# Performance work log

Hardware: AMD Instinct MI355X
Metric: run time of the kernel (lower is better)

The kernel has to match this reference:

```python
import jax, jax.numpy as jnp
import numpy as np

ROI = 7  # roi_size


def _conv1x1_softmax_fuse(a, b, w, bias):
    # a, b: (..., C, H, W); w: (2, 2C); bias: (2,)
    cat = jnp.concatenate([a, b], axis=-3)
    logits = jnp.einsum('oc,...chw->...ohw', w, cat) + bias[:, None, None]
    att = jax.nn.softmax(logits, axis=-3)
    return a * att[..., 0:1, :, :] + b * att[..., 1:2, :, :]


def _roi_align(feat, anchors):
    # torchvision RoIAlign (aligned=False, spatial_scale=1, sampling_ratio=-1).
    # Box width == ROI exactly -> bin size 1, adaptive grid = 1 sample per bin
    # at bin center: sample point = anchor - ROI/2 + (p + 0.5), p in [0, ROI).
    # feat: (C,H,W), anchors: (N,2) -> (N,C,ROI,ROI)
    C, H, W = feat.shape
    N = anchors.shape[0]
    half = ROI / 2.0
    offs = jnp.arange(ROI, dtype=feat.dtype) + 0.5
    sx = anchors[:, 0, None] - half + offs  # (N, ROI)
    sy = anchors[:, 1, None] - half + offs
    X = jnp.broadcast_to(sx[:, None, :], (N, ROI, ROI)).reshape(-1)  # pw fastest
    Y = jnp.broadcast_to(sy[:, :, None], (N, ROI, ROI)).reshape(-1)
    valid = (X >= -1.0) & (X <= W) & (Y >= -1.0) & (Y <= H)
    x = jnp.maximum(X, 0.0)
    y = jnp.maximum(Y, 0.0)
    x0 = jnp.floor(x).astype(jnp.int32)
    y0 = jnp.floor(y).astype(jnp.int32)
    xl = jnp.minimum(x0, W - 1)
    xh = jnp.minimum(x0 + 1, W - 1)
    yl = jnp.minimum(y0, H - 1)
    yh = jnp.minimum(y0 + 1, H - 1)
    lx = jnp.where(x0 >= W - 1, 0.0, x - xl)
    ly = jnp.where(y0 >= H - 1, 0.0, y - yl)
    hx, hy = 1.0 - lx, 1.0 - ly
    v = (feat[:, yl, xl] * (hy * hx) + feat[:, yl, xh] * (hy * lx)
         + feat[:, yh, xl] * (ly * hx) + feat[:, yh, xh] * (ly * lx))  # (C, P)
    v = jnp.where(valid, v, 0.0)
    return v.reshape(C, N, ROI, ROI).transpose(1, 0, 2, 3)


def _scatter_rois(base, rois, x0, y0):
    # sequential per-anchor overwrite of ROIxROI patches, matching torch loop order
    def step(m, args):
        roi, xx, yy = args
        return jax.lax.dynamic_update_slice(m, roi, (0, yy, xx)), None
    out, _ = jax.lax.scan(step, base, (rois, x0, y0))
    return out


def _forward(feat_rgb, feat_tir, a_rgb_c, a_tir_c, w_global, b_global, w_att, b_att):
    anchors_rgb = jax.lax.stop_gradient(a_rgb_c[..., :2])
    anchors_tir = jax.lax.stop_gradient(a_tir_c[..., :2])
    # GlobalFeatureFusion == per-pixel 1x1 conv + softmax-2 blend
    fused_global = _conv1x1_softmax_fuse(feat_rgb, feat_tir, w_global, b_global)
    rgb_rois = jax.vmap(_roi_align)(feat_rgb, anchors_rgb)  # (B,N,C,r,r)
    tir_rois = jax.vmap(_roi_align)(feat_tir, anchors_tir)
    fused_rois = _conv1x1_softmax_fuse(rgb_rois, tir_rois, w_att, b_att)
    fused_rois = jax.lax.stop_gradient(fused_rois)  # .detach() in fuse_rois_to_map
    H, W = feat_rgb.shape[2], feat_rgb.shape[3]
    half = ROI / 2.0
    x0 = jnp.clip(jnp.trunc(anchors_rgb[..., 0] - half).astype(jnp.int32), 0, W - ROI)
    y0 = jnp.clip(jnp.trunc(anchors_rgb[..., 1] - half).astype(jnp.int32), 0, H - ROI)
    return jax.vmap(_scatter_rois)(fused_global, fused_rois, x0, y0)


def setup_inputs():
    key = jax.random.key(0)
    ks = jax.random.split(key, 10)
    B, C, H, W, N = 8, 256, 128, 128, 128
    half = ROI / 2.0
    feat_rgb = jax.random.normal(ks[0], (B, C, H, W), dtype=jnp.float32)
    feat_tir = jax.random.normal(ks[1], (B, C, H, W), dtype=jnp.float32)

    def anchors(kx, ky, kc):
        ax = jax.random.uniform(kx, (B, N), minval=half, maxval=W - half)
        ay = jax.random.uniform(ky, (B, N), minval=half, maxval=H - half)
        cf = jax.random.uniform(kc, (B, N))
        return jnp.stack([ax, ay, cf], axis=-1).astype(jnp.float32)

    a_rgb = anchors(ks[2], ks[3], ks[4])
    a_tir = anchors(ks[5], ks[6], ks[7])
    w_global = jax.random.normal(ks[8], (2, 2 * C), dtype=jnp.float32) * 0.05
    b_global = jnp.zeros((2,), dtype=jnp.float32)
    w_att = jax.random.normal(ks[9], (2, 2 * C), dtype=jnp.float32) * 0.05
    b_att = jnp.zeros((2,), dtype=jnp.float32)
    return {"feat_rgb": feat_rgb, "feat_tir": feat_tir,
            "anchors_rgb_with_conf": a_rgb, "anchors_tir_with_conf": a_tir,
            "w_global": w_global, "b_global": b_global,
            "w_att": w_att, "b_att": b_att}


def reference(feat_rgb, feat_tir, anchors_rgb_with_conf, anchors_tir_with_conf,
              w_global, b_global, w_att, b_att):
    return _forward(feat_rgb, feat_tir, anchors_rgb_with_conf, anchors_tir_with_conf,
                    w_global, b_global, w_att, b_att)
```

## Files before the change

### kernel.cpp

```cpp
#include <hip/hip_runtime.h>
#include <math.h>

#define ROI 7
#define NC 256
#define TC 512
#define HH 128
#define WW 128
#define HW (HH * WW)

__global__ void init_owner_k(int* __restrict__ owner, int n) {
    int i = blockIdx.x * blockDim.x + threadIdx.x;
    if (i < n) owner[i] = -1;
}

__global__ void mark_owner_k(const float* __restrict__ anchors,
                             int* __restrict__ owner, int B, int N) {
    int i = blockIdx.x * blockDim.x + threadIdx.x;
    int total = B * N * 49;
    if (i >= total) return;
    int p = i % 49;
    int bn = i / 49;
    int n = bn % N;
    int b = bn / N;
    float ax = anchors[(size_t)(b * N + n) * 3 + 0];
    float ay = anchors[(size_t)(b * N + n) * 3 + 1];
    int x0 = (int)truncf(ax - 3.5f); x0 = min(max(x0, 0), WW - ROI);
    int y0 = (int)truncf(ay - 3.5f); y0 = min(max(y0, 0), HH - ROI);
    int x = x0 + (p % 7);
    int y = y0 + (p / 7);
    atomicMax(&owner[((size_t)b << 14) + (y << 7) + x], n);
}

__global__ __launch_bounds__(512, 4) void fuse_global_k(
        const float* __restrict__ rgb, const float* __restrict__ tir,
        const float* __restrict__ wg, const float* __restrict__ bg,
        const int* __restrict__ owner, float* __restrict__ out) {
    __shared__ float w[2 * TC];
    __shared__ float part0[64][9];
    __shared__ float part1[64][9];
    __shared__ float att[64];

    int tid = threadIdx.x;
    int px = tid & 63;
    int g  = tid >> 6;
    int b = blockIdx.x >> 8;
    int pix = ((blockIdx.x & 255) << 6) + px;

    for (int i = tid; i < 2 * TC; i += 512) w[i] = wg[i];

    bool act = owner[((size_t)b << 14) + pix] < 0;

    const float* pr = rgb + (((size_t)b * NC) << 14) + pix;
    const float* pt = tir + (((size_t)b * NC) << 14) + pix;
    int c0 = g << 5;

    __syncthreads();

    float vr[32], vt[32];
    if (act) {
        float l0 = 0.f, l1 = 0.f;
        #pragma unroll
        for (int i = 0; i < 32; ++i) {
            int c = c0 + i;
            vr[i] = pr[(size_t)c << 14];
            vt[i] = pt[(size_t)c << 14];
            l0 = fmaf(w[c],          vr[i], fmaf(w[NC + c],     vt[i], l0));
            l1 = fmaf(w[2 * NC + c], vr[i], fmaf(w[3 * NC + c], vt[i], l1));
        }
        part0[px][g] = l0;
        part1[px][g] = l1;
    }
    __syncthreads();
    if (g == 0 && act) {
        float L0 = bg[0], L1 = bg[1];
        #pragma unroll
        for (int s = 0; s < 8; ++s) { L0 += part0[px][s]; L1 += part1[px][s]; }
        float m = fmaxf(L0, L1);
        float e0 = expf(L0 - m), e1 = expf(L1 - m);
        att[px] = e0 / (e0 + e1);
    }
    __syncthreads();
    if (!act) return;

    float a0 = att[px];
    float* po = out + (((size_t)b * NC) << 14) + pix;
    #pragma unroll
    for (int i = 0; i < 32; ++i) {
        int c = c0 + i;
        po[(size_t)c << 14] = fmaf(a0, vr[i] - vt[i], vt[i]);
    }
}

struct Bilin { int o00, o01, o10, o11; float w00, w01, w10, w11; };

__device__ inline Bilin bilin_setup(float X, float Y) {
    Bilin r;
    bool valid = (X >= -1.0f) && (X <= (float)WW) && (Y >= -1.0f) && (Y <= (float)HH);
    float x = fmaxf(X, 0.0f), y = fmaxf(Y, 0.0f);
    int ix = (int)floorf(x), iy = (int)floorf(y);
    int xl = min(ix, WW - 1), xh = min(ix + 1, WW - 1);
    int yl = min(iy, HH - 1), yh = min(iy + 1, HH - 1);
    float lx = (ix >= WW - 1) ? 0.0f : x - (float)xl;
    float ly = (iy >= HH - 1) ? 0.0f : y - (float)yl;
    float hx = 1.0f - lx, hy = 1.0f - ly;
    r.o00 = (yl << 7) + xl; r.o01 = (yl << 7) + xh;
    r.o10 = (yh << 7) + xl; r.o11 = (yh << 7) + xh;
    float s = valid ? 1.0f : 0.0f;
    r.w00 = hy * hx * s; r.w01 = hy * lx * s;
    r.w10 = ly * hx * s; r.w11 = ly * lx * s;
    return r;
}

__device__ inline float bgather(const float* __restrict__ base, int c, const Bilin& bl) {
    const float* p = base + ((size_t)c << 14);
    return p[bl.o00] * bl.w00 + p[bl.o01] * bl.w01 +
           p[bl.o10] * bl.w10 + p[bl.o11] * bl.w11;
}

__global__ __launch_bounds__(512) void roi_scatter_k(
        const float* __restrict__ rgb, const float* __restrict__ tir,
        const float* __restrict__ a_rgb, const float* __restrict__ a_tir,
        const float* __restrict__ wa, const float* __restrict__ ba,
        const int* __restrict__ owner, float* __restrict__ out, int N, int B) {
    __shared__ float w[2 * TC];
    __shared__ float part0[64][9];
    __shared__ float part1[64][9];
    __shared__ float att0s[64];

    int bid = blockIdx.x;
    int b = (B - 1) - bid / N;
    int n = bid % N;
    for (int i = threadIdx.x; i < 2 * TC; i += 512) w[i] = wa[i];

    int p = threadIdx.x & 63;
    int g = threadIdx.x >> 6;
    int px = p % 7, py = p / 7;

    float axr = a_rgb[(size_t)(b * N + n) * 3 + 0];
    float ayr = a_rgb[(size_t)(b * N + n) * 3 + 1];
    float axt = a_tir[(size_t)(b * N + n) * 3 + 0];
    float ayt = a_tir[(size_t)(b * N + n) * 3 + 1];

    int x0 = (int)truncf(axr - 3.5f); x0 = min(max(x0, 0), WW - ROI);
    int y0 = (int)truncf(ayr - 3.5f); y0 = min(max(y0, 0), HH - ROI);
    int x = x0 + px, y = y0 + py;

    bool act = (p < 49);
    if (act) act = (owner[((size_t)b << 14) + (y << 7) + x] == n);

    Bilin br = bilin_setup(axr - 3.0f + (float)px, ayr - 3.0f + (float)py);
    Bilin bt = bilin_setup(axt - 3.0f + (float)px, ayt - 3.0f + (float)py);

    const float* rb = rgb + (((size_t)b * NC) << 14);
    const float* tb = tir + (((size_t)b * NC) << 14);

    __syncthreads();

    int c0 = g << 5;
    float vr[32], vt[32];
    if (act) {
        float l0 = 0.f, l1 = 0.f;
        #pragma unroll
        for (int i = 0; i < 32; ++i) {
            int c = c0 + i;
            vr[i] = bgather(rb, c, br);
            vt[i] = bgather(tb, c, bt);
            l0 = fmaf(w[c],          vr[i], fmaf(w[NC + c],     vt[i], l0));
            l1 = fmaf(w[2 * NC + c], vr[i], fmaf(w[3 * NC + c], vt[i], l1));
        }
        part0[p][g] = l0;
        part1[p][g] = l1;
    }
    __syncthreads();
    if (g == 0 && p < 49) {
        float L0 = ba[0], L1 = ba[1];
        #pragma unroll
        for (int s = 0; s < 8; ++s) { L0 += part0[p][s]; L1 += part1[p][s]; }
        float m = fmaxf(L0, L1);
        float e0 = expf(L0 - m), e1 = expf(L1 - m);
        att0s[p] = e0 / (e0 + e1);
    }
    __syncthreads();
    if (!act) return;

    float a0 = att0s[p];
    float* po = out + (((size_t)b * NC) << 14) + (y << 7) + x;
    #pragma unroll
    for (int i = 0; i < 32; ++i) {
        int c = c0 + i;
        po[(size_t)c << 14] = fmaf(a0, vr[i] - vt[i], vt[i]);
    }
}

extern "C" void kernel_launch(void* const* d_in, const int* in_sizes, int n_in,
                              void* d_out, int out_size, void* d_ws, size_t ws_size,
                              hipStream_t stream) {
    const float* frgb = (const float*)d_in[0];
    const float* ftir = (const float*)d_in[1];
    const float* argb = (const float*)d_in[2];
    const float* atir = (const float*)d_in[3];
    const float* wg   = (const float*)d_in[4];
    const float* bgp  = (const float*)d_in[5];
    const float* wa   = (const float*)d_in[6];
    const float* bap  = (const float*)d_in[7];
    float* out = (float*)d_out;

    int B = in_sizes[0] / (NC * HW);
    int N = in_sizes[2] / (B * 3);
    int npix = B * HW;

    int* owner = (int*)d_ws;

    init_owner_k<<<(npix + 255) / 256, 256, 0, stream>>>(owner, npix);
    mark_owner_k<<<(B * N * 49 + 255) / 256, 256, 0, stream>>>(argb, owner, B, N);
    fuse_global_k<<<npix / 64, 512, 0, stream>>>(frgb, ftir, wg, bgp, owner, out);
    roi_scatter_k<<<B * N, 512, 0, stream>>>(frgb, ftir, argb, atir, wa, bap,
                                             owner, out, N, B);
}
```

Measured before the change: 223.6 us.

## Merge global fuse and ROI scatter kernels into one interleaved launch

Combines the global 1x1 fusion kernel and the ROI scatter kernel into a single launch whose blocks are dispatched as either ROI or global-fuse work. When the fuse block count is twice the ROI count, ROI blocks are interleaved one in three, so the gather-heavy ROI blocks overlap with the streaming fuse blocks rather than running as a separate tail. This removes one kernel launch and the serialization between them. In exchange, the merged kernel loses the fuse kernel's min-blocks launch bound hint, which may change register allocation and occupancy.

```diff
diff --git a/kernel.cpp b/kernel.cpp
--- a/kernel.cpp
+++ b/kernel.cpp
@@ -31,66 +31,6 @@
     atomicMax(&owner[((size_t)b << 14) + (y << 7) + x], n);
 }
 
-__global__ __launch_bounds__(512, 4) void fuse_global_k(
-        const float* __restrict__ rgb, const float* __restrict__ tir,
-        const float* __restrict__ wg, const float* __restrict__ bg,
-        const int* __restrict__ owner, float* __restrict__ out) {
-    __shared__ float w[2 * TC];
-    __shared__ float part0[64][9];
-    __shared__ float part1[64][9];
-    __shared__ float att[64];
-
-    int tid = threadIdx.x;
-    int px = tid & 63;
-    int g  = tid >> 6;
-    int b = blockIdx.x >> 8;
-    int pix = ((blockIdx.x & 255) << 6) + px;
-
-    for (int i = tid; i < 2 * TC; i += 512) w[i] = wg[i];
-
-    bool act = owner[((size_t)b << 14) + pix] < 0;
-
-    const float* pr = rgb + (((size_t)b * NC) << 14) + pix;
-    const float* pt = tir + (((size_t)b * NC) << 14) + pix;
-    int c0 = g << 5;
-
-    __syncthreads();
-
-    float vr[32], vt[32];
-    if (act) {
-        float l0 = 0.f, l1 = 0.f;
-        #pragma unroll
-        for (int i = 0; i < 32; ++i) {
-            int c = c0 + i;
-            vr[i] = pr[(size_t)c << 14];
-            vt[i] = pt[(size_t)c << 14];
-            l0 = fmaf(w[c],          vr[i], fmaf(w[NC + c],     vt[i], l0));
-            l1 = fmaf(w[2 * NC + c], vr[i], fmaf(w[3 * NC + c], vt[i], l1));
-        }
-        part0[px][g] = l0;
-        part1[px][g] = l1;
-    }
-    __syncthreads();
-    if (g == 0 && act) {
-        float L0 = bg[0], L1 = bg[1];
-        #pragma unroll
-        for (int s = 0; s < 8; ++s) { L0 += part0[px][s]; L1 += part1[px][s]; }
-        float m = fmaxf(L0, L1);
-        float e0 = expf(L0 - m), e1 = expf(L1 - m);
-        att[px] = e0 / (e0 + e1);
-    }
-    __syncthreads();
-    if (!act) return;
-
-    float a0 = att[px];
-    float* po = out + (((size_t)b * NC) << 14) + pix;
-    #pragma unroll
-    for (int i = 0; i < 32; ++i) {
-        int c = c0 + i;
-        po[(size_t)c << 14] = fmaf(a0, vr[i] - vt[i], vt[i]);
-    }
-}
-
 struct Bilin { int o00, o01, o10, o11; float w00, w01, w10, w11; };
 
 __device__ inline Bilin bilin_setup(float X, float Y) {
@@ -117,78 +57,140 @@
            p[bl.o10] * bl.w10 + p[bl.o11] * bl.w11;
 }
 
-__global__ __launch_bounds__(512) void roi_scatter_k(
+__global__ __launch_bounds__(512) void fused_k(
         const float* __restrict__ rgb, const float* __restrict__ tir,
         const float* __restrict__ a_rgb, const float* __restrict__ a_tir,
+        const float* __restrict__ wg, const float* __restrict__ bg,
         const float* __restrict__ wa, const float* __restrict__ ba,
-        const int* __restrict__ owner, float* __restrict__ out, int N, int B) {
+        const int* __restrict__ owner, float* __restrict__ out,
+        int N, int nRoi, int nFuse) {
     __shared__ float w[2 * TC];
     __shared__ float part0[64][9];
     __shared__ float part1[64][9];
-    __shared__ float att0s[64];
+    __shared__ float att[64];
 
     int bid = blockIdx.x;
-    int b = (B - 1) - bid / N;
-    int n = bid % N;
-    for (int i = threadIdx.x; i < 2 * TC; i += 512) w[i] = wa[i];
-
-    int p = threadIdx.x & 63;
-    int g = threadIdx.x >> 6;
-    int px = p % 7, py = p / 7;
-
-    float axr = a_rgb[(size_t)(b * N + n) * 3 + 0];
-    float ayr = a_rgb[(size_t)(b * N + n) * 3 + 1];
-    float axt = a_tir[(size_t)(b * N + n) * 3 + 0];
-    float ayt = a_tir[(size_t)(b * N + n) * 3 + 1];
-
-    int x0 = (int)truncf(axr - 3.5f); x0 = min(max(x0, 0), WW - ROI);
-    int y0 = (int)truncf(ayr - 3.5f); y0 = min(max(y0, 0), HH - ROI);
-    int x = x0 + px, y = y0 + py;
-
-    bool act = (p < 49);
-    if (act) act = (owner[((size_t)b << 14) + (y << 7) + x] == n);
-
-    Bilin br = bilin_setup(axr - 3.0f + (float)px, ayr - 3.0f + (float)py);
-    Bilin bt = bilin_setup(axt - 3.0f + (float)px, ayt - 3.0f + (float)py);
-
-    const float* rb = rgb + (((size_t)b * NC) << 14);
-    const float* tb = tir + (((size_t)b * NC) << 14);
-
-    __syncthreads();
-
+    int tid = threadIdx.x;
+
+    bool isRoi;
+    int idx;
+    if (nFuse == 2 * nRoi) {
+        int q = bid / 3, r = bid - 3 * q;
+        isRoi = (r == 0);
+        idx = isRoi ? q : (bid - q - 1);
+    } else {
+        isRoi = (bid < nRoi);
+        idx = isRoi ? bid : (bid - nRoi);
+    }
+
+    int p  = tid & 63;
+    int g  = tid >> 6;
     int c0 = g << 5;
-    float vr[32], vt[32];
-    if (act) {
-        float l0 = 0.f, l1 = 0.f;
+
+    if (isRoi) {
+        int b = idx / N, n = idx % N;
+        for (int i = tid; i < 2 * TC; i += 512) w[i] = wa[i];
+
+        int px = p % 7, py = p / 7;
+
+        float axr = a_rgb[(size_t)(b * N + n) * 3 + 0];
+        float ayr = a_rgb[(size_t)(b * N + n) * 3 + 1];
+        float axt = a_tir[(size_t)(b * N + n) * 3 + 0];
+        float ayt = a_tir[(size_t)(b * N + n) * 3 + 1];
+
+        int x0 = (int)truncf(axr - 3.5f); x0 = min(max(x0, 0), WW - ROI);
+        int y0 = (int)truncf(ayr - 3.5f); y0 = min(max(y0, 0), HH - ROI);
+        int x = x0 + px, y = y0 + py;
+
+        bool act = (p < 49);
+        if (act) act = (owner[((size_t)b << 14) + (y << 7) + x] == n);
+
+        Bilin br = bilin_setup(axr - 3.0f + (float)px, ayr - 3.0f + (float)py);
+        Bilin bt = bilin_setup(axt - 3.0f + (float)px, ayt - 3.0f + (float)py);
+
+        const float* rb = rgb + (((size_t)b * NC) << 14);
+        const float* tb = tir + (((size_t)b * NC) << 14);
+
+        __syncthreads();
+
+        float vr[32], vt[32];
+        if (act) {
+            float l0 = 0.f, l1 = 0.f;
+            #pragma unroll
+            for (int i = 0; i < 32; ++i) {
+                int c = c0 + i;
+                vr[i] = bgather(rb, c, br);
+                vt[i] = bgather(tb, c, bt);
+                l0 = fmaf(w[c],          vr[i], fmaf(w[NC + c],     vt[i], l0));
+                l1 = fmaf(w[2 * NC + c], vr[i], fmaf(w[3 * NC + c], vt[i], l1));
+            }
+            part0[p][g] = l0;
+            part1[p][g] = l1;
+        }
+        __syncthreads();
+        if (g == 0 && p < 49) {
+            float L0 = ba[0], L1 = ba[1];
+            #pragma unroll
+            for (int s = 0; s < 8; ++s) { L0 += part0[p][s]; L1 += part1[p][s]; }
+            float m = fmaxf(L0, L1);
+            float e0 = expf(L0 - m), e1 = expf(L1 - m);
+            att[p] = e0 / (e0 + e1);
+        }
+        __syncthreads();
+        if (!act) return;
+
+        float a0 = att[p];
+        float* po = out + (((size_t)b * NC) << 14) + (y << 7) + x;
         #pragma unroll
         for (int i = 0; i < 32; ++i) {
             int c = c0 + i;
-            vr[i] = bgather(rb, c, br);
-            vt[i] = bgather(tb, c, bt);
-            l0 = fmaf(w[c],          vr[i], fmaf(w[NC + c],     vt[i], l0));
-            l1 = fmaf(w[2 * NC + c], vr[i], fmaf(w[3 * NC + c], vt[i], l1));
-        }
-        part0[p][g] = l0;
-        part1[p][g] = l1;
-    }
-    __syncthreads();
-    if (g == 0 && p < 49) {
-        float L0 = ba[0], L1 = ba[1];
+            po[(size_t)c << 14] = fmaf(a0, vr[i] - vt[i], vt[i]);
+        }
+    } else {
+        int b = idx >> 8;
+        int pix = ((idx & 255) << 6) + p;
+        for (int i = tid; i < 2 * TC; i += 512) w[i] = wg[i];
+
+        bool act = owner[((size_t)b << 14) + pix] < 0;
+
+        const float* pr = rgb + (((size_t)b * NC) << 14) + pix;
+        const float* pt = tir + (((size_t)b * NC) << 14) + pix;
+
+        __syncthreads();
+
+        float vr[32], vt[32];
+        if (act) {
+            float l0 = 0.f, l1 = 0.f;
+            #pragma unroll
+            for (int i = 0; i < 32; ++i) {
+                int c = c0 + i;
+                vr[i] = pr[(size_t)c << 14];
+                vt[i] = pt[(size_t)c << 14];
+                l0 = fmaf(w[c],          vr[i], fmaf(w[NC + c],     vt[i], l0));
+                l1 = fmaf(w[2 * NC + c], vr[i], fmaf(w[3 * NC + c], vt[i], l1));
+            }
+            part0[p][g] = l0;
+            part1[p][g] = l1;
+        }
+        __syncthreads();
+        if (g == 0 && act) {
+            float L0 = bg[0], L1 = bg[1];
+            #pragma unroll
+            for (int s = 0; s < 8; ++s) { L0 += part0[p][s]; L1 += part1[p][s]; }
+            float m = fmaxf(L0, L1);
+            float e0 = expf(L0 - m), e1 = expf(L1 - m);
+            att[p] = e0 / (e0 + e1);
+        }
+        __syncthreads();
+        if (!act) return;
+
+        float a0 = att[p];
+        float* po = out + (((size_t)b * NC) << 14) + pix;
         #pragma unroll
-        for (int s = 0; s < 8; ++s) { L0 += part0[p][s]; L1 += part1[p][s]; }
-        float m = fmaxf(L0, L1);
-        float e0 = expf(L0 - m), e1 = expf(L1 - m);
-        att0s[p] = e0 / (e0 + e1);
-    }
-    __syncthreads();
-    if (!act) return;
-
-    float a0 = att0s[p];
-    float* po = out + (((size_t)b * NC) << 14) + (y << 7) + x;
-    #pragma unroll
-    for (int i = 0; i < 32; ++i) {
-        int c = c0 + i;
-        po[(size_t)c << 14] = fmaf(a0, vr[i] - vt[i], vt[i]);
+        for (int i = 0; i < 32; ++i) {
+            int c = c0 + i;
+            po[(size_t)c << 14] = fmaf(a0, vr[i] - vt[i], vt[i]);
+        }
     }
 }
 
@@ -208,12 +210,14 @@
     int B = in_sizes[0] / (NC * HW);
     int N = in_sizes[2] / (B * 3);
     int npix = B * HW;
+    int nRoi = B * N;
+    int nFuse = npix / 64;
 
     int* owner = (int*)d_ws;
 
     init_owner_k<<<(npix + 255) / 256, 256, 0, stream>>>(owner, npix);
     mark_owner_k<<<(B * N * 49 + 255) / 256, 256, 0, stream>>>(argb, owner, B, N);
-    fuse_global_k<<<npix / 64, 512, 0, stream>>>(frgb, ftir, wg, bgp, owner, out);
-    roi_scatter_k<<<B * N, 512, 0, stream>>>(frgb, ftir, argb, atir, wa, bap,
-                                             owner, out, N, B);
-}
+    fused_k<<<nRoi + nFuse, 512, 0, stream>>>(frgb, ftir, argb, atir,
+                                              wg, bgp, wa, bap,
+                                              owner, out, N, nRoi, nFuse);
+}
```

New measurement: 196.1 us. -12.3%, faster.
